# Optimization experiments

Hardware: AMD Instinct MI355X
Metric: run time of the kernel (lower is better)

The kernel has to match this reference:

```python
import jax, jax.numpy as jnp
import numpy as np

N_NODES = 100000
N_GRAPHS = 512
IN_CH, HID, OUT_CH = 128, 32, 10
N_EDGES = 3200000


def gcn_conv(x, src, dst, norm, W, b, n_nodes):
    # h = X W  (transform first: PyG GCNConv does lin() before propagate)
    h = x @ W                                   # [N, F_out]
    # gather source features, scale by symmetric norm, scatter-add to targets
    msgs = h[src] * norm[:, None]               # [E+N, F_out]
    out = jax.ops.segment_sum(msgs, dst, num_segments=n_nodes)
    return out + b


def _sym_norm(edge_index, n_nodes):
    # add self-loops, compute D^{-1/2} (A+I) D^{-1/2} edge weights
    loops = jnp.arange(n_nodes, dtype=edge_index.dtype)
    src = jnp.concatenate([edge_index[0], loops])
    dst = jnp.concatenate([edge_index[1], loops])
    deg = jax.ops.segment_sum(jnp.ones_like(dst, dtype=jnp.float32), dst,
                              num_segments=n_nodes)
    dinv = jnp.where(deg > 0, jax.lax.rsqrt(jnp.maximum(deg, 1.0)), 0.0)
    norm = dinv[src] * dinv[dst]
    return src, dst, norm


def setup_inputs() -> dict:
    key = jax.random.key(0)
    ks = jax.random.split(key, 12)
    x = jax.random.normal(ks[0], (N_NODES, IN_CH), dtype=jnp.float32)
    edge_index = jax.random.randint(ks[1], (2, N_EDGES), 0, N_NODES, dtype=jnp.int64)
    batch = jnp.sort(jax.random.randint(ks[2], (N_NODES,), 0, N_GRAPHS, dtype=jnp.int64))
    def glorot(k, fi, fo):
        lim = np.sqrt(6.0 / (fi + fo)).astype(np.float32)
        return jax.random.uniform(k, (fi, fo), jnp.float32, -lim, lim)
    return {
        "x": x, "edge_index": edge_index, "batch": batch,
        "W1": glorot(ks[3], IN_CH, HID), "b1": jnp.zeros((HID,), jnp.float32),
        "W2": glorot(ks[4], HID, HID),   "b2": jnp.zeros((HID,), jnp.float32),
        "W3": glorot(ks[5], HID, HID),   "b3": jnp.zeros((HID,), jnp.float32),
        "Wl": glorot(ks[6], HID, OUT_CH), "bl": jnp.zeros((OUT_CH,), jnp.float32),
    }


def reference(x, edge_index, batch, W1, b1, W2, b2, W3, b3, Wl, bl):
    n_nodes = x.shape[0]
    src, dst, norm = _sym_norm(edge_index, n_nodes)
    h = gcn_conv(x, src, dst, norm, W1, b1, n_nodes)
    h = jax.nn.relu(h)
    h = gcn_conv(h, src, dst, norm, W2, b2, n_nodes)
    h = jax.nn.relu(h)
    h = gcn_conv(h, src, dst, norm, W3, b3, n_nodes)  # no relu on last layer
    # global mean pool over graphs in the batch
    sums = jax.ops.segment_sum(h, batch, num_segments=N_GRAPHS)   # [G, HID]
    cnts = jax.ops.segment_sum(jnp.ones((n_nodes,), jnp.float32), batch,
                               num_segments=N_GRAPHS)
    emb = sums / jnp.maximum(cnts, 1.0)[:, None]
    # dropout(p=0.5) is identity in eval mode
    return emb @ Wl + bl
```

## Files before the change

### kernel.cpp

```cpp
#include <hip/hip_runtime.h>
#include <hip/hip_bf16.h>
#include <hip/hip_fp16.h>

#define N_NODES  100000
#define N_GRAPHS 512
#define IN_CH    128
#define HID      32
#define OUT_CH   10
#define N_EDGES  3200000

#define SZC   256
#define NBC   ((N_NODES + SZC - 1) / SZC)
#define CAPC  9216
#define RND   8192
#define BKT   1024
#define EPT   8
#define NRND  ((N_EDGES + RND - 1) / RND)

typedef _Float16 half8 __attribute__((ext_vector_type(8)));
typedef float    f32x4 __attribute__((ext_vector_type(4)));

__device__ __forceinline__ int load_idx(const int* __restrict__ p, long long pos, int is64) {
  return is64 ? p[2 * pos] : p[(int)pos];
}

__device__ __forceinline__ void h8_acc(float4 raw, float* a) {
  const __half2* ph = (const __half2*)&raw;
#pragma unroll
  for (int q = 0; q < 4; q++) {
    float2 f = __half22float2(ph[q]);
    a[2 * q]     += f.x;
    a[2 * q + 1] += f.y;
  }
}

__global__ void detect_i64(const int* __restrict__ ei, const int* __restrict__ batch,
                           int* __restrict__ flag) {
  __shared__ int any_nz;
  const int* buf = (blockIdx.x == 0) ? ei : batch;
  if (threadIdx.x == 0) any_nz = 0;
  __syncthreads();
  for (int i = threadIdx.x; i < 4096; i += 256) {
    if (buf[2 * i + 1] != 0) any_nz = 1;
  }
  __syncthreads();
  if (threadIdx.x == 0) flag[blockIdx.x] = any_nz ? 0 : 1;
}

__global__ void pack_w(const float* __restrict__ W1, const float* __restrict__ W2,
                       const float* __restrict__ W3, __half* __restrict__ P1,
                       __half* __restrict__ P2, __half* __restrict__ P3) {
  int t = threadIdx.x;
  for (int idx = t; idx < 4 * 2 * 64 * 8; idx += 256) {
    int j = idx & 7, l = (idx >> 3) & 63, ct = (idx >> 9) & 1, s = idx >> 10;
    int k = s * 32 + (l >> 4) * 8 + j, c = ct * 16 + (l & 15);
    P1[idx] = __float2half(W1[k * 32 + c]);
  }
  for (int idx = t; idx < 2 * 64 * 8; idx += 256) {
    int j = idx & 7, l = (idx >> 3) & 63, ct = (idx >> 9) & 1;
    int k = (l >> 4) * 8 + j, c = ct * 16 + (l & 15);
    P2[idx] = __float2half(W2[k * 32 + c]);
    P3[idx] = __float2half(W3[k * 32 + c]);
  }
}

__global__ void bucket_k(const int* __restrict__ ei, const int* __restrict__ flag,
                         int* __restrict__ gcur, int* __restrict__ bstore) {
  __shared__ int hist[NBC];
  __shared__ int base[NBC];
  int is64 = flag[0];
  int t = threadIdx.x;
  int rd = blockIdx.x;
  for (int i = t; i < NBC; i += BKT) hist[i] = 0;
  __syncthreads();
  long long e0 = (long long)rd * RND;
  int   pk[EPT];
  short cb[EPT];
#pragma unroll
  for (int k = 0; k < EPT; k++) {
    long long e = e0 + k * BKT + t;
    if (e < N_EDGES) {
      int s = load_idx(ei, e, is64);
      int d = load_idx(ei, N_EDGES + e, is64);
      pk[k] = (s << 8) | (d & 255);
      cb[k] = (short)(d >> 8);
      atomicAdd(&hist[d >> 8], 1);
    } else {
      cb[k] = -1;
    }
  }
  __syncthreads();
  for (int c = t; c < NBC; c += BKT) {
    int h = hist[c];
    if (h > 0) base[c] = atomicAdd(&gcur[c], h);
  }
  __syncthreads();
#pragma unroll
  for (int k = 0; k < EPT; k++) {
    if (cb[k] >= 0) {
      int c = cb[k];
      int pos = atomicAdd(&base[c], 1);
      if (pos < CAPC) bstore[(size_t)c * CAPC + pos] = pk[k];
    }
  }
}

__global__ void bscan_k(const int* __restrict__ gcur, int* __restrict__ bbase) {
  __shared__ int part[256];
  int t = threadIdx.x;
  const int CHUNK = (NBC + 255) / 256;
  int v[CHUNK];
  int s = 0;
  int base = t * CHUNK;
  for (int k = 0; k < CHUNK; k++) {
    int i = base + k;
    v[k] = (i < NBC) ? min(gcur[i], CAPC) : 0;
    s += v[k];
  }
  part[t] = s;
  __syncthreads();
  if (t == 0) {
    int run = 0;
    for (int i = 0; i < 256; i++) { int x = part[i]; part[i] = run; run += x; }
  }
  __syncthreads();
  int run = part[t];
  for (int k = 0; k < CHUNK; k++) {
    int i = base + k;
    if (i < NBC) bbase[i] = run;
    run += v[k];
  }
}

__global__ void build_csr(const int* __restrict__ bstore, const int* __restrict__ gcur,
                          const int* __restrict__ bbase, int* __restrict__ csr,
                          int* __restrict__ row_ptr, int* __restrict__ deg,
                          float* __restrict__ dinv) {
  __shared__ int hist[SZC];
  __shared__ int sc[SZC];
  __shared__ int cur[SZC];
  int b = blockIdx.x, t = threadIdx.x;
  hist[t] = 0;
  __syncthreads();
  int cnt = min(gcur[b], CAPC);
  const int* eb = bstore + (size_t)b * CAPC;
  for (int i = t; i < cnt; i += 256) atomicAdd(&hist[eb[i] & 255], 1);
  __syncthreads();
  int own = hist[t];
  sc[t] = own;
  __syncthreads();
  for (int off = 1; off < SZC; off <<= 1) {
    int u = (t >= off) ? sc[t - off] : 0;
    __syncthreads();
    sc[t] += u;
    __syncthreads();
  }
  int excl = sc[t] - own;
  int gbase = bbase[b];
  int node = b * SZC + t;
  if (node < N_NODES) {
    row_ptr[node] = gbase + excl;
    deg[node]     = own;
    dinv[node]    = rsqrtf((float)(own + 1));
  }
  cur[t] = excl;
  __syncthreads();
  for (int i = t; i < cnt; i += 256) {
    int pk = eb[i];
    int pos = atomicAdd(&cur[pk & 255], 1);
    csr[gbase + pos] = pk >> 8;
  }
}

template <int K>
__global__ void gemm_mfma(const float* __restrict__ X, const __half* __restrict__ P,
                          const float* __restrict__ dinv, __half* __restrict__ G) {
  int wid  = threadIdx.x >> 6;
  int lane = threadIdx.x & 63;
  int row0 = (blockIdx.x * 4 + wid) * 16;
  if (row0 >= N_NODES) return;
  int r  = lane & 15;
  int ko = lane >> 4;
  f32x4 acc0 = {0.f, 0.f, 0.f, 0.f};
  f32x4 acc1 = {0.f, 0.f, 0.f, 0.f};
  const float* xrow = X + (size_t)(row0 + r) * K + ko * 8;
#pragma unroll
  for (int s = 0; s < K / 32; s++) {
    float4 xa = *(const float4*)(xrow + s * 32);
    float4 xb = *(const float4*)(xrow + s * 32 + 4);
    half8 a;
    a[0] = (_Float16)xa.x; a[1] = (_Float16)xa.y;
    a[2] = (_Float16)xa.z; a[3] = (_Float16)xa.w;
    a[4] = (_Float16)xb.x; a[5] = (_Float16)xb.y;
    a[6] = (_Float16)xb.z; a[7] = (_Float16)xb.w;
    half8 b0 = *(const half8*)(P + ((size_t)(s * 2 + 0) * 64 + lane) * 8);
    half8 b1 = *(const half8*)(P + ((size_t)(s * 2 + 1) * 64 + lane) * 8);
    acc0 = __builtin_amdgcn_mfma_f32_16x16x32_f16(a, b0, acc0, 0, 0, 0);
    acc1 = __builtin_amdgcn_mfma_f32_16x16x32_f16(a, b1, acc1, 0, 0, 0);
  }
  int col   = lane & 15;
  int rbase = row0 + (lane >> 4) * 4;
#pragma unroll
  for (int i = 0; i < 4; i++) {
    float dn = dinv[rbase + i];
    G[(size_t)(rbase + i) * 32 + col]      = __float2half(acc0[i] * dn);
    G[(size_t)(rbase + i) * 32 + 16 + col] = __float2half(acc1[i] * dn);
  }
}

__global__ void agg_pull(const __half* __restrict__ g, const int* __restrict__ csr,
                         const int* __restrict__ row_ptr, const int* __restrict__ deg,
                         const float* __restrict__ dinv, const float* __restrict__ bias,
                         float* __restrict__ out, int do_relu) {
  int node = blockIdx.x * 32 + (threadIdx.x >> 3);
  if (node >= N_NODES) return;
  int half = (threadIdx.x >> 2) & 1;
  int j    = threadIdx.x & 3;
  const __half* gj = g + j * 8;
  int start = row_ptr[node];
  int dn = deg[node];
  float a0[8] = {0.f, 0.f, 0.f, 0.f, 0.f, 0.f, 0.f, 0.f};
  float a1[8] = {0.f, 0.f, 0.f, 0.f, 0.f, 0.f, 0.f, 0.f};
  float a2[8] = {0.f, 0.f, 0.f, 0.f, 0.f, 0.f, 0.f, 0.f};
  float a3[8] = {0.f, 0.f, 0.f, 0.f, 0.f, 0.f, 0.f, 0.f};
  int i = half;
  for (; i + 6 < dn; i += 8) {
    int s0 = csr[start + i];
    int s1 = csr[start + i + 2];
    int s2 = csr[start + i + 4];
    int s3 = csr[start + i + 6];
    float4 r0 = *(const float4*)(gj + (size_t)s0 * HID);
    float4 r1 = *(const float4*)(gj + (size_t)s1 * HID);
    float4 r2 = *(const float4*)(gj + (size_t)s2 * HID);
    float4 r3 = *(const float4*)(gj + (size_t)s3 * HID);
    h8_acc(r0, a0);
    h8_acc(r1, a1);
    h8_acc(r2, a2);
    h8_acc(r3, a3);
  }
  for (; i < dn; i += 2) {
    int s0 = csr[start + i];
    h8_acc(*(const float4*)(gj + (size_t)s0 * HID), a0);
  }
#pragma unroll
  for (int k = 0; k < 8; k++) a0[k] += a1[k] + a2[k] + a3[k];
#pragma unroll
  for (int k = 0; k < 8; k++) a0[k] += __shfl_xor(a0[k], 4, 64);
  if (half == 0) {
    float self[8] = {0.f, 0.f, 0.f, 0.f, 0.f, 0.f, 0.f, 0.f};
    h8_acc(*(const float4*)(gj + (size_t)node * HID), self);
    float dnv = dinv[node];
    float4 bb0 = *(const float4*)(bias + j * 8);
    float4 bb1 = *(const float4*)(bias + j * 8 + 4);
    float bbv[8] = {bb0.x, bb0.y, bb0.z, bb0.w, bb1.x, bb1.y, bb1.z, bb1.w};
    float r[8];
#pragma unroll
    for (int k = 0; k < 8; k++) {
      r[k] = dnv * (a0[k] + self[k]) + bbv[k];
      if (do_relu) r[k] = fmaxf(r[k], 0.f);
    }
    *(float4*)(out + (size_t)node * HID + j * 8)     = make_float4(r[0], r[1], r[2], r[3]);
    *(float4*)(out + (size_t)node * HID + j * 8 + 4) = make_float4(r[4], r[5], r[6], r[7]);
  }
}

__global__ void pool_head(const float* __restrict__ h, const int* __restrict__ batch,
                          const int* __restrict__ flag, const float* __restrict__ Wl,
                          const float* __restrict__ bl, float* __restrict__ out) {
  __shared__ float acc[8][HID];
  int g = blockIdx.x, t = threadIdx.x;
  int is64 = flag[1];
  int start, end;
  {
    int lo = 0, hi = N_NODES;
    while (lo < hi) { int m = (lo + hi) >> 1; if (load_idx(batch, m, is64) < g) lo = m + 1; else hi = m; }
    start = lo;
    lo = start; hi = N_NODES;
    while (lo < hi) { int m = (lo + hi) >> 1; if (load_idx(batch, m, is64) < g + 1) lo = m + 1; else hi = m; }
    end = lo;
  }
  int c = t & 31, r = t >> 5;
  float s = 0.f;
  for (int i = start + r; i < end; i += 8) s += h[(size_t)i * HID + c];
  acc[r][c] = s;
  __syncthreads();
  if (t < HID) {
    float v = 0.f;
#pragma unroll
    for (int q = 0; q < 8; q++) v += acc[q][t];
    acc[0][t] = v / fmaxf((float)(end - start), 1.0f);
  }
  __syncthreads();
  if (t < OUT_CH) {
    float o = bl[t];
#pragma unroll
    for (int k = 0; k < HID; k++) o += acc[0][k] * Wl[k * OUT_CH + t];
    out[g * OUT_CH + t] = o;
  }
}

extern "C" void kernel_launch(void* const* d_in, const int* in_sizes, int n_in,
                              void* d_out, int out_size, void* d_ws, size_t ws_size,
                              hipStream_t stream) {
  const float* x   = (const float*)d_in[0];
  const int* ei    = (const int*)d_in[1];
  const int* batch = (const int*)d_in[2];
  const float* W1  = (const float*)d_in[3];
  const float* b1  = (const float*)d_in[4];
  const float* W2  = (const float*)d_in[5];
  const float* b2  = (const float*)d_in[6];
  const float* W3  = (const float*)d_in[7];
  const float* b3  = (const float*)d_in[8];
  const float* Wl  = (const float*)d_in[9];
  const float* bl  = (const float*)d_in[10];
  float* out = (float*)d_out;

  char* p = (char*)d_ws;
  auto alloc = [&](size_t bytes) {
    void* r = (void*)p;
    p += (bytes + 255) & ~(size_t)255;
    return r;
  };
  int*    gcur    = (int*)alloc((size_t)NBC * 4);
  int*    bbase   = (int*)alloc((size_t)NBC * 4);
  int*    bstore  = (int*)alloc((size_t)NBC * CAPC * 4);
  int*    csr     = (int*)alloc((size_t)N_EDGES * 4);
  int*    row_ptr = (int*)alloc((size_t)N_NODES * 4);
  int*    deg     = (int*)alloc((size_t)N_NODES * 4);
  float*  dinv    = (float*)alloc((size_t)N_NODES * 4);
  int*    flag    = (int*)alloc(8);
  __half* g       = (__half*)alloc((size_t)N_NODES * HID * 2);
  float*  h       = (float*)alloc((size_t)N_NODES * HID * 4);
  __half* P1      = (__half*)alloc((size_t)4 * 2 * 64 * 8 * 2);
  __half* P2      = (__half*)alloc((size_t)2 * 64 * 8 * 2);
  __half* P3      = (__half*)alloc((size_t)2 * 64 * 8 * 2);

  hipMemsetAsync(gcur, 0, (size_t)NBC * 4, stream);

  detect_i64<<<2, 256, 0, stream>>>(ei, batch, flag);
  pack_w<<<1, 256, 0, stream>>>(W1, W2, W3, P1, P2, P3);
  bucket_k<<<NRND, BKT, 0, stream>>>(ei, flag, gcur, bstore);
  bscan_k<<<1, 256, 0, stream>>>(gcur, bbase);
  build_csr<<<NBC, 256, 0, stream>>>(bstore, gcur, bbase, csr, row_ptr, deg, dinv);

  const int GB = (N_NODES / 16 + 3) / 4;
  const int AB = (N_NODES + 31) / 32;
  gemm_mfma<IN_CH><<<GB, 256, 0, stream>>>(x, P1, dinv, g);
  agg_pull<<<AB, 256, 0, stream>>>(g, csr, row_ptr, deg, dinv, b1, h, 1);
  gemm_mfma<HID><<<GB, 256, 0, stream>>>(h, P2, dinv, g);
  agg_pull<<<AB, 256, 0, stream>>>(g, csr, row_ptr, deg, dinv, b2, h, 1);
  gemm_mfma<HID><<<GB, 256, 0, stream>>>(h, P3, dinv, g);
  agg_pull<<<AB, 256, 0, stream>>>(g, csr, row_ptr, deg, dinv, b3, h, 0);

  pool_head<<<N_GRAPHS, 256, 0, stream>>>(h, batch, flag, Wl, bl, out);
}
```

Measured before the change: 237.5 us.

## Split neighbor aggregation into two source-range passes for cache locality

After: 241.7 us. About the same (+1.8%).

```diff
diff --git a/kernel.cpp b/kernel.cpp
--- a/kernel.cpp
+++ b/kernel.cpp
@@ -8,6 +8,7 @@
 #define HID      32
 #define OUT_CH   10
 #define N_EDGES  3200000
+#define SPLIT    50000
 
 #define SZC   256
 #define NBC   ((N_NODES + SZC - 1) / SZC)
@@ -49,8 +50,10 @@
 
 __global__ void pack_w(const float* __restrict__ W1, const float* __restrict__ W2,
                        const float* __restrict__ W3, __half* __restrict__ P1,
-                       __half* __restrict__ P2, __half* __restrict__ P3) {
+                       __half* __restrict__ P2, __half* __restrict__ P3,
+                       int* __restrict__ gcur) {
   int t = threadIdx.x;
+  for (int i = t; i < NBC; i += 256) gcur[i] = 0;
   for (int idx = t; idx < 4 * 2 * 64 * 8; idx += 256) {
     int j = idx & 7, l = (idx >> 3) & 63, ct = (idx >> 9) & 1, s = idx >> 10;
     int k = s * 32 + (l >> 4) * 8 + j, c = ct * 16 + (l & 15);
@@ -135,18 +138,24 @@
 __global__ void build_csr(const int* __restrict__ bstore, const int* __restrict__ gcur,
                           const int* __restrict__ bbase, int* __restrict__ csr,
                           int* __restrict__ row_ptr, int* __restrict__ deg,
-                          float* __restrict__ dinv) {
-  __shared__ int hist[SZC];
+                          int* __restrict__ deg_lo, float* __restrict__ dinv) {
+  __shared__ int hist[2 * SZC];
   __shared__ int sc[SZC];
-  __shared__ int cur[SZC];
+  __shared__ int cur[2 * SZC];
   int b = blockIdx.x, t = threadIdx.x;
   hist[t] = 0;
+  hist[t + 256] = 0;
   __syncthreads();
   int cnt = min(gcur[b], CAPC);
   const int* eb = bstore + (size_t)b * CAPC;
-  for (int i = t; i < cnt; i += 256) atomicAdd(&hist[eb[i] & 255], 1);
-  __syncthreads();
-  int own = hist[t];
+  for (int i = t; i < cnt; i += 256) {
+    int pk = eb[i];
+    int key = ((pk & 255) << 1) | ((pk >> 8) >= SPLIT ? 1 : 0);
+    atomicAdd(&hist[key], 1);
+  }
+  __syncthreads();
+  int lo = hist[2 * t], hi = hist[2 * t + 1];
+  int own = lo + hi;
   sc[t] = own;
   __syncthreads();
   for (int off = 1; off < SZC; off <<= 1) {
@@ -161,13 +170,16 @@
   if (node < N_NODES) {
     row_ptr[node] = gbase + excl;
     deg[node]     = own;
+    deg_lo[node]  = lo;
     dinv[node]    = rsqrtf((float)(own + 1));
   }
-  cur[t] = excl;
+  cur[2 * t]     = excl;
+  cur[2 * t + 1] = excl + lo;
   __syncthreads();
   for (int i = t; i < cnt; i += 256) {
     int pk = eb[i];
-    int pos = atomicAdd(&cur[pk & 255], 1);
+    int key = ((pk & 255) << 1) | ((pk >> 8) >= SPLIT ? 1 : 0);
+    int pos = atomicAdd(&cur[key], 1);
     csr[gbase + pos] = pk >> 8;
   }
 }
@@ -208,9 +220,11 @@
   }
 }
 
+template <int PASS>
 __global__ void agg_pull(const __half* __restrict__ g, const int* __restrict__ csr,
                          const int* __restrict__ row_ptr, const int* __restrict__ deg,
-                         const float* __restrict__ dinv, const float* __restrict__ bias,
+                         const int* __restrict__ deg_lo, const float* __restrict__ dinv,
+                         const float* __restrict__ bias, float* __restrict__ partial,
                          float* __restrict__ out, int do_relu) {
   int node = blockIdx.x * 32 + (threadIdx.x >> 3);
   if (node >= N_NODES) return;
@@ -218,17 +232,20 @@
   int j    = threadIdx.x & 3;
   const __half* gj = g + j * 8;
   int start = row_ptr[node];
-  int dn = deg[node];
+  int dl    = deg_lo[node];
+  int base, n;
+  if (PASS == 0) { base = start;      n = dl; }
+  else           { base = start + dl; n = deg[node] - dl; }
   float a0[8] = {0.f, 0.f, 0.f, 0.f, 0.f, 0.f, 0.f, 0.f};
   float a1[8] = {0.f, 0.f, 0.f, 0.f, 0.f, 0.f, 0.f, 0.f};
   float a2[8] = {0.f, 0.f, 0.f, 0.f, 0.f, 0.f, 0.f, 0.f};
   float a3[8] = {0.f, 0.f, 0.f, 0.f, 0.f, 0.f, 0.f, 0.f};
   int i = half;
-  for (; i + 6 < dn; i += 8) {
-    int s0 = csr[start + i];
-    int s1 = csr[start + i + 2];
-    int s2 = csr[start + i + 4];
-    int s3 = csr[start + i + 6];
+  for (; i + 6 < n; i += 8) {
+    int s0 = csr[base + i];
+    int s1 = csr[base + i + 2];
+    int s2 = csr[base + i + 4];
+    int s3 = csr[base + i + 6];
     float4 r0 = *(const float4*)(gj + (size_t)s0 * HID);
     float4 r1 = *(const float4*)(gj + (size_t)s1 * HID);
     float4 r2 = *(const float4*)(gj + (size_t)s2 * HID);
@@ -238,8 +255,8 @@
     h8_acc(r2, a2);
     h8_acc(r3, a3);
   }
-  for (; i < dn; i += 2) {
-    int s0 = csr[start + i];
+  for (; i < n; i += 2) {
+    int s0 = csr[base + i];
     h8_acc(*(const float4*)(gj + (size_t)s0 * HID), a0);
   }
 #pragma unroll
@@ -247,20 +264,28 @@
 #pragma unroll
   for (int k = 0; k < 8; k++) a0[k] += __shfl_xor(a0[k], 4, 64);
   if (half == 0) {
-    float self[8] = {0.f, 0.f, 0.f, 0.f, 0.f, 0.f, 0.f, 0.f};
-    h8_acc(*(const float4*)(gj + (size_t)node * HID), self);
-    float dnv = dinv[node];
-    float4 bb0 = *(const float4*)(bias + j * 8);
-    float4 bb1 = *(const float4*)(bias + j * 8 + 4);
-    float bbv[8] = {bb0.x, bb0.y, bb0.z, bb0.w, bb1.x, bb1.y, bb1.z, bb1.w};
-    float r[8];
-#pragma unroll
-    for (int k = 0; k < 8; k++) {
-      r[k] = dnv * (a0[k] + self[k]) + bbv[k];
-      if (do_relu) r[k] = fmaxf(r[k], 0.f);
+    if (PASS == 0) {
+      *(float4*)(partial + (size_t)node * HID + j * 8)     = make_float4(a0[0], a0[1], a0[2], a0[3]);
+      *(float4*)(partial + (size_t)node * HID + j * 8 + 4) = make_float4(a0[4], a0[5], a0[6], a0[7]);
+    } else {
+      float4 p0 = *(const float4*)(partial + (size_t)node * HID + j * 8);
+      float4 p1 = *(const float4*)(partial + (size_t)node * HID + j * 8 + 4);
+      float pv[8] = {p0.x, p0.y, p0.z, p0.w, p1.x, p1.y, p1.z, p1.w};
+      float self[8] = {0.f, 0.f, 0.f, 0.f, 0.f, 0.f, 0.f, 0.f};
+      h8_acc(*(const float4*)(gj + (size_t)node * HID), self);
+      float dnv = dinv[node];
+      float4 bb0 = *(const float4*)(bias + j * 8);
+      float4 bb1 = *(const float4*)(bias + j * 8 + 4);
+      float bbv[8] = {bb0.x, bb0.y, bb0.z, bb0.w, bb1.x, bb1.y, bb1.z, bb1.w};
+      float r[8];
+#pragma unroll
+      for (int k = 0; k < 8; k++) {
+        r[k] = dnv * (a0[k] + pv[k] + self[k]) + bbv[k];
+        if (do_relu) r[k] = fmaxf(r[k], 0.f);
+      }
+      *(float4*)(out + (size_t)node * HID + j * 8)     = make_float4(r[0], r[1], r[2], r[3]);
+      *(float4*)(out + (size_t)node * HID + j * 8 + 4) = make_float4(r[4], r[5], r[6], r[7]);
     }
-    *(float4*)(out + (size_t)node * HID + j * 8)     = make_float4(r[0], r[1], r[2], r[3]);
-    *(float4*)(out + (size_t)node * HID + j * 8 + 4) = make_float4(r[4], r[5], r[6], r[7]);
   }
 }
 
@@ -327,6 +352,7 @@
   int*    csr     = (int*)alloc((size_t)N_EDGES * 4);
   int*    row_ptr = (int*)alloc((size_t)N_NODES * 4);
   int*    deg     = (int*)alloc((size_t)N_NODES * 4);
+  int*    deg_lo  = (int*)alloc((size_t)N_NODES * 4);
   float*  dinv    = (float*)alloc((size_t)N_NODES * 4);
   int*    flag    = (int*)alloc(8);
   __half* g       = (__half*)alloc((size_t)N_NODES * HID * 2);
@@ -334,23 +360,25 @@
   __half* P1      = (__half*)alloc((size_t)4 * 2 * 64 * 8 * 2);
   __half* P2      = (__half*)alloc((size_t)2 * 64 * 8 * 2);
   __half* P3      = (__half*)alloc((size_t)2 * 64 * 8 * 2);
-
-  hipMemsetAsync(gcur, 0, (size_t)NBC * 4, stream);
+  float*  partial = (float*)bstore;
 
   detect_i64<<<2, 256, 0, stream>>>(ei, batch, flag);
-  pack_w<<<1, 256, 0, stream>>>(W1, W2, W3, P1, P2, P3);
+  pack_w<<<1, 256, 0, stream>>>(W1, W2, W3, P1, P2, P3, gcur);
   bucket_k<<<NRND, BKT, 0, stream>>>(ei, flag, gcur, bstore);
   bscan_k<<<1, 256, 0, stream>>>(gcur, bbase);
-  build_csr<<<NBC, 256, 0, stream>>>(bstore, gcur, bbase, csr, row_ptr, deg, dinv);
+  build_csr<<<NBC, 256, 0, stream>>>(bstore, gcur, bbase, csr, row_ptr, deg, deg_lo, dinv);
 
   const int GB = (N_NODES / 16 + 3) / 4;
   const int AB = (N_NODES + 31) / 32;
   gemm_mfma<IN_CH><<<GB, 256, 0, stream>>>(x, P1, dinv, g);
-  agg_pull<<<AB, 256, 0, stream>>>(g, csr, row_ptr, deg, dinv, b1, h, 1);
+  agg_pull<0><<<AB, 256, 0, stream>>>(g, csr, row_ptr, deg, deg_lo, dinv, b1, partial, h, 0);
+  agg_pull<1><<<AB, 256, 0, stream>>>(g, csr, row_ptr, deg, deg_lo, dinv, b1, partial, h, 1);
   gemm_mfma<HID><<<GB, 256, 0, stream>>>(h, P2, dinv, g);
-  agg_pull<<<AB, 256, 0, stream>>>(g, csr, row_ptr, deg, dinv, b2, h, 1);
+  agg_pull<0><<<AB, 256, 0, stream>>>(g, csr, row_ptr, deg, deg_lo, dinv, b2, partial, h, 0);
+  agg_pull<1><<<AB, 256, 0, stream>>>(g, csr, row_ptr, deg, deg_lo, dinv, b2, partial, h, 1);
   gemm_mfma<HID><<<GB, 256, 0, stream>>>(h, P3, dinv, g);
-  agg_pull<<<AB, 256, 0, stream>>>(g, csr, row_ptr, deg, dinv, b3, h, 0);
+  agg_pull<0><<<AB, 256, 0, stream>>>(g, csr, row_ptr, deg, deg_lo, dinv, b3, partial, h, 0);
+  agg_pull<1><<<AB, 256, 0, stream>>>(g, csr, row_ptr, deg, deg_lo, dinv, b3, partial, h, 0);
 
   pool_head<<<N_GRAPHS, 256, 0, stream>>>(h, batch, flag, Wl, bl, out);
 }
```

## Use fixed-slab padded CSR to drop bucket scan and vectorize index loads

Applied to the files above, without the earlier changes.

Result: faster. 230.0 us (-3.1%).

```diff
diff --git a/kernel.cpp b/kernel.cpp
--- a/kernel.cpp
+++ b/kernel.cpp
@@ -12,6 +12,7 @@
 #define SZC   256
 #define NBC   ((N_NODES + SZC - 1) / SZC)
 #define CAPC  9216
+#define SLAB  10240
 #define RND   8192
 #define BKT   1024
 #define EPT   8
@@ -49,8 +50,10 @@
 
 __global__ void pack_w(const float* __restrict__ W1, const float* __restrict__ W2,
                        const float* __restrict__ W3, __half* __restrict__ P1,
-                       __half* __restrict__ P2, __half* __restrict__ P3) {
+                       __half* __restrict__ P2, __half* __restrict__ P3,
+                       int* __restrict__ gcur) {
   int t = threadIdx.x;
+  for (int i = t; i < NBC; i += 256) gcur[i] = 0;
   for (int idx = t; idx < 4 * 2 * 64 * 8; idx += 256) {
     int j = idx & 7, l = (idx >> 3) & 63, ct = (idx >> 9) & 1, s = idx >> 10;
     int k = s * 32 + (l >> 4) * 8 + j, c = ct * 16 + (l & 15);
@@ -105,37 +108,9 @@
   }
 }
 
-__global__ void bscan_k(const int* __restrict__ gcur, int* __restrict__ bbase) {
-  __shared__ int part[256];
-  int t = threadIdx.x;
-  const int CHUNK = (NBC + 255) / 256;
-  int v[CHUNK];
-  int s = 0;
-  int base = t * CHUNK;
-  for (int k = 0; k < CHUNK; k++) {
-    int i = base + k;
-    v[k] = (i < NBC) ? min(gcur[i], CAPC) : 0;
-    s += v[k];
-  }
-  part[t] = s;
-  __syncthreads();
-  if (t == 0) {
-    int run = 0;
-    for (int i = 0; i < 256; i++) { int x = part[i]; part[i] = run; run += x; }
-  }
-  __syncthreads();
-  int run = part[t];
-  for (int k = 0; k < CHUNK; k++) {
-    int i = base + k;
-    if (i < NBC) bbase[i] = run;
-    run += v[k];
-  }
-}
-
 __global__ void build_csr(const int* __restrict__ bstore, const int* __restrict__ gcur,
-                          const int* __restrict__ bbase, int* __restrict__ csr,
-                          int* __restrict__ row_ptr, int* __restrict__ deg,
-                          float* __restrict__ dinv) {
+                          int* __restrict__ csr, int* __restrict__ row_ptr,
+                          int* __restrict__ deg, float* __restrict__ dinv) {
   __shared__ int hist[SZC];
   __shared__ int sc[SZC];
   __shared__ int cur[SZC];
@@ -147,7 +122,8 @@
   for (int i = t; i < cnt; i += 256) atomicAdd(&hist[eb[i] & 255], 1);
   __syncthreads();
   int own = hist[t];
-  sc[t] = own;
+  int pd  = (own + 3) & ~3;
+  sc[t] = pd;
   __syncthreads();
   for (int off = 1; off < SZC; off <<= 1) {
     int u = (t >= off) ? sc[t - off] : 0;
@@ -155,8 +131,8 @@
     sc[t] += u;
     __syncthreads();
   }
-  int excl = sc[t] - own;
-  int gbase = bbase[b];
+  int excl = sc[t] - pd;
+  int gbase = b * SLAB;
   int node = b * SZC + t;
   if (node < N_NODES) {
     row_ptr[node] = gbase + excl;
@@ -217,33 +193,32 @@
   int half = (threadIdx.x >> 2) & 1;
   int j    = threadIdx.x & 3;
   const __half* gj = g + j * 8;
-  int start = row_ptr[node];
-  int dn = deg[node];
+  int base = row_ptr[node];
+  int n    = deg[node];
+  int nh   = ((n >> 1) + 3) & ~3;
+  if (nh > n) nh = n;
+  int lo = half ? nh : 0;
+  int hi = half ? n : nh;
   float a0[8] = {0.f, 0.f, 0.f, 0.f, 0.f, 0.f, 0.f, 0.f};
   float a1[8] = {0.f, 0.f, 0.f, 0.f, 0.f, 0.f, 0.f, 0.f};
-  float a2[8] = {0.f, 0.f, 0.f, 0.f, 0.f, 0.f, 0.f, 0.f};
-  float a3[8] = {0.f, 0.f, 0.f, 0.f, 0.f, 0.f, 0.f, 0.f};
-  int i = half;
-  for (; i + 6 < dn; i += 8) {
-    int s0 = csr[start + i];
-    int s1 = csr[start + i + 2];
-    int s2 = csr[start + i + 4];
-    int s3 = csr[start + i + 6];
-    float4 r0 = *(const float4*)(gj + (size_t)s0 * HID);
-    float4 r1 = *(const float4*)(gj + (size_t)s1 * HID);
-    float4 r2 = *(const float4*)(gj + (size_t)s2 * HID);
-    float4 r3 = *(const float4*)(gj + (size_t)s3 * HID);
+  int i = lo;
+  for (; i + 3 < hi; i += 4) {
+    int4 s4 = *(const int4*)(csr + base + i);
+    float4 r0 = *(const float4*)(gj + (size_t)s4.x * HID);
+    float4 r1 = *(const float4*)(gj + (size_t)s4.y * HID);
+    float4 r2 = *(const float4*)(gj + (size_t)s4.z * HID);
+    float4 r3 = *(const float4*)(gj + (size_t)s4.w * HID);
     h8_acc(r0, a0);
     h8_acc(r1, a1);
-    h8_acc(r2, a2);
-    h8_acc(r3, a3);
-  }
-  for (; i < dn; i += 2) {
-    int s0 = csr[start + i];
+    h8_acc(r2, a0);
+    h8_acc(r3, a1);
+  }
+  for (; i < hi; i++) {
+    int s0 = csr[base + i];
     h8_acc(*(const float4*)(gj + (size_t)s0 * HID), a0);
   }
 #pragma unroll
-  for (int k = 0; k < 8; k++) a0[k] += a1[k] + a2[k] + a3[k];
+  for (int k = 0; k < 8; k++) a0[k] += a1[k];
 #pragma unroll
   for (int k = 0; k < 8; k++) a0[k] += __shfl_xor(a0[k], 4, 64);
   if (half == 0) {
@@ -322,9 +297,8 @@
     return r;
   };
   int*    gcur    = (int*)alloc((size_t)NBC * 4);
-  int*    bbase   = (int*)alloc((size_t)NBC * 4);
   int*    bstore  = (int*)alloc((size_t)NBC * CAPC * 4);
-  int*    csr     = (int*)alloc((size_t)N_EDGES * 4);
+  int*    csr     = (int*)alloc((size_t)NBC * SLAB * 4);
   int*    row_ptr = (int*)alloc((size_t)N_NODES * 4);
   int*    deg     = (int*)alloc((size_t)N_NODES * 4);
   float*  dinv    = (float*)alloc((size_t)N_NODES * 4);
@@ -335,13 +309,10 @@
   __half* P2      = (__half*)alloc((size_t)2 * 64 * 8 * 2);
   __half* P3      = (__half*)alloc((size_t)2 * 64 * 8 * 2);
 
-  hipMemsetAsync(gcur, 0, (size_t)NBC * 4, stream);
-
   detect_i64<<<2, 256, 0, stream>>>(ei, batch, flag);
-  pack_w<<<1, 256, 0, stream>>>(W1, W2, W3, P1, P2, P3);
+  pack_w<<<1, 256, 0, stream>>>(W1, W2, W3, P1, P2, P3, gcur);
   bucket_k<<<NRND, BKT, 0, stream>>>(ei, flag, gcur, bstore);
-  bscan_k<<<1, 256, 0, stream>>>(gcur, bbase);
-  build_csr<<<NBC, 256, 0, stream>>>(bstore, gcur, bbase, csr, row_ptr, deg, dinv);
+  build_csr<<<NBC, 256, 0, stream>>>(bstore, gcur, csr, row_ptr, deg, dinv);
 
   const int GB = (N_NODES / 16 + 3) / 4;
   const int AB = (N_NODES + 31) / 32;
```
